# Optimization experiments

Hardware: AMD Instinct MI355X
Metric: run time of the kernel (lower is better)

Reference implementation:

```python
import jax, jax.numpy as jnp
import numpy as np

N_NODES = 50000
N_EDGES = 1600000
N_GRAPHS = 64


def setup_inputs() -> dict:
    key = jax.random.key(0)
    ks = jax.random.split(key, 16)
    p = lambda k, shape: (jax.random.normal(k, shape, dtype=jnp.float32) * 0.05)
    x = jax.random.normal(ks[0], (N_NODES, 128), dtype=jnp.float32)
    edge_index = jax.random.randint(ks[1], (2, N_EDGES), 0, N_NODES, dtype=jnp.int32)
    edge_attr = jax.random.uniform(ks[2], (N_EDGES,), dtype=jnp.float32)
    batch = jnp.sort(jax.random.randint(ks[3], (N_NODES,), 0, N_GRAPHS, dtype=jnp.int32))
    return {
        'x': x, 'edge_index': edge_index, 'edge_attr': edge_attr, 'batch': batch,
        'W1': p(ks[4], (128, 128)), 'b1': jnp.zeros((128,), jnp.float32),
        'W2': p(ks[5], (128, 64)), 'b2': jnp.zeros((64,), jnp.float32),
        'gW1': p(ks[6], (64, 32)), 'gb1': jnp.zeros((32,), jnp.float32),
        'gW2': p(ks[7], (32, 1)), 'gb2': jnp.zeros((1,), jnp.float32),
        'fcW1': p(ks[8], (64, 128)), 'fcb1': jnp.zeros((128,), jnp.float32),
        'fcW2': p(ks[9], (128, 2)), 'fcb2': jnp.zeros((2,), jnp.float32),
    }


def gcn_conv(x, src, dst, ew, W, b):
    # PyG GCNConv with edge weights: add self-loops (weight 1), symmetric norm.
    xw = x @ W  # [N, out]
    deg = jax.ops.segment_sum(ew, dst, num_segments=N_NODES) + 1.0  # self-loop
    dinv = jnp.where(deg > 0, jax.lax.rsqrt(deg), 0.0)
    coef = dinv[src] * ew * dinv[dst]  # [E]
    agg = jax.ops.segment_sum(coef[:, None] * xw[src], dst, num_segments=N_NODES)
    agg = agg + (dinv * dinv)[:, None] * xw  # self-loop contribution
    return agg + b


def global_attention(x, batch, gW1, gb1, gW2, gb2):
    # gate_nn: Linear(64,32)->ReLU->Linear(32,1), segment-softmax over graphs
    g = (jax.nn.relu(x @ gW1 + gb1) @ gW2 + gb2)[:, 0]  # [N]
    gmax = jax.ops.segment_max(g, batch, num_segments=N_GRAPHS)
    ex = jnp.exp(g - gmax[batch])
    den = jax.ops.segment_sum(ex, batch, num_segments=N_GRAPHS)
    alpha = ex / den[batch]
    return jax.ops.segment_sum(alpha[:, None] * x, batch, num_segments=N_GRAPHS)


def reference(x, edge_index, edge_attr, batch, W1, b1, W2, b2,
              gW1, gb1, gW2, gb2, fcW1, fcb1, fcW2, fcb2):
    src, dst = edge_index[0], edge_index[1]
    h = jax.nn.relu(gcn_conv(x, src, dst, edge_attr, W1, b1))
    x1 = jax.nn.relu(gcn_conv(h, src, dst, edge_attr, W2, b2))
    x2 = global_attention(x1, batch, gW1, gb1, gW2, gb2)  # [G, 64]
    # dropout is identity in eval mode
    h2 = jax.nn.relu(x2 @ fcW1 + fcb1)
    logits = h2 @ fcW2 + fcb2
    return jax.nn.log_softmax(logits, axis=1)
```

## Files before the change

### kernel.cpp

```cpp
#include <hip/hip_runtime.h>
#include <hip/hip_bf16.h>
#include <hip/hip_fp16.h>

#define N_NODES 50000
#define N_EDGES 1600000
#define N_GRAPHS 64
#define G1BLKS 1563

__device__ __forceinline__ unsigned fenc(float x) {
    unsigned u = __float_as_uint(x);
    return (u & 0x80000000u) ? ~u : (u | 0x80000000u);
}
__device__ __forceinline__ float fdec(unsigned e) {
    return (e & 0x80000000u) ? __uint_as_float(e & 0x7fffffffu) : __uint_as_float(~e);
}
__device__ __forceinline__ float ew_of(unsigned p) {
    return __half2float(__ushort_as_half((unsigned short)(p & 0xFFFFu)));
}

__global__ void mega1(const float* __restrict__ X, const float* __restrict__ W,
                      __half* __restrict__ Yh, const int* __restrict__ dst,
                      int* __restrict__ cnt, int* __restrict__ pos) {
    __shared__ float Xl[32][132];
    if (blockIdx.x >= G1BLKS) {
        int e = (blockIdx.x - G1BLKS) * 256 + threadIdx.x;
        if (e < N_EDGES) pos[e] = atomicAdd(&cnt[dst[e]], 1);
        return;
    }
    const int rt = threadIdx.x >> 5;
    const int ct = threadIdx.x & 31;
    const int base = blockIdx.x * 32;
    for (int i = threadIdx.x; i < 32 * 32; i += 256) {
        int rr = i >> 5, cc = (i & 31) << 2;
        int gr = base + rr;
        float4 v = (gr < N_NODES) ? *(const float4*)&X[(size_t)gr * 128 + cc]
                                  : make_float4(0.f, 0.f, 0.f, 0.f);
        Xl[rr][cc] = v.x; Xl[rr][cc + 1] = v.y; Xl[rr][cc + 2] = v.z; Xl[rr][cc + 3] = v.w;
    }
    __syncthreads();
    float acc[4][4] = {};
    for (int k = 0; k < 128; k += 4) {
        float4 a0 = *(const float4*)&Xl[rt * 4 + 0][k];
        float4 a1 = *(const float4*)&Xl[rt * 4 + 1][k];
        float4 a2 = *(const float4*)&Xl[rt * 4 + 2][k];
        float4 a3 = *(const float4*)&Xl[rt * 4 + 3][k];
        float4 w0 = *(const float4*)&W[(size_t)(k + 0) * 128 + ct * 4];
        float4 w1 = *(const float4*)&W[(size_t)(k + 1) * 128 + ct * 4];
        float4 w2 = *(const float4*)&W[(size_t)(k + 2) * 128 + ct * 4];
        float4 w3 = *(const float4*)&W[(size_t)(k + 3) * 128 + ct * 4];
        #define STEP(av, wv)  \
            acc[0][0] += av##0 * wv.x; acc[0][1] += av##0 * wv.y; acc[0][2] += av##0 * wv.z; acc[0][3] += av##0 * wv.w; \
            acc[1][0] += av##1 * wv.x; acc[1][1] += av##1 * wv.y; acc[1][2] += av##1 * wv.z; acc[1][3] += av##1 * wv.w; \
            acc[2][0] += av##2 * wv.x; acc[2][1] += av##2 * wv.y; acc[2][2] += av##2 * wv.z; acc[2][3] += av##2 * wv.w; \
            acc[3][0] += av##3 * wv.x; acc[3][1] += av##3 * wv.y; acc[3][2] += av##3 * wv.z; acc[3][3] += av##3 * wv.w;
        { float ax0=a0.x, ax1=a1.x, ax2=a2.x, ax3=a3.x; STEP(ax, w0) }
        { float ay0=a0.y, ay1=a1.y, ay2=a2.y, ay3=a3.y; STEP(ay, w1) }
        { float az0=a0.z, az1=a1.z, az2=a2.z, az3=a3.z; STEP(az, w2) }
        { float aw0=a0.w, aw1=a1.w, aw2=a2.w, aw3=a3.w; STEP(aw, w3) }
        #undef STEP
    }
    const int pc = ct >> 3;
    const int cw = (ct & 7) * 4;
    for (int i = 0; i < 4; ++i) {
        int gr = base + rt * 4 + i;
        if (gr < N_NODES) {
            ushort4 u;
            u.x = __half_as_ushort(__float2half(acc[i][0]));
            u.y = __half_as_ushort(__float2half(acc[i][1]));
            u.z = __half_as_ushort(__float2half(acc[i][2]));
            u.w = __half_as_ushort(__float2half(acc[i][3]));
            *(ushort4*)&Yh[((size_t)pc * N_NODES + gr) * 32 + cw] = u;
        }
    }
}

__global__ void block_sums(const int* __restrict__ cnt, int* __restrict__ bsum) {
    __shared__ int s[256];
    int idx = blockIdx.x * 256 + threadIdx.x;
    s[threadIdx.x] = (idx < N_NODES) ? cnt[idx] : 0;
    __syncthreads();
    for (int o = 128; o; o >>= 1) {
        if (threadIdx.x < o) s[threadIdx.x] += s[threadIdx.x + o];
        __syncthreads();
    }
    if (threadIdx.x == 0) bsum[blockIdx.x] = s[0];
}

__global__ void scan_bsums(const int* __restrict__ bsum, int* __restrict__ boff,
                           int nb, int* __restrict__ row_start_last) {
    __shared__ int s[256];
    int v = (threadIdx.x < nb) ? bsum[threadIdx.x] : 0;
    s[threadIdx.x] = v;
    __syncthreads();
    for (int o = 1; o < 256; o <<= 1) {
        int t = 0;
        if (threadIdx.x >= o) t = s[threadIdx.x - o];
        __syncthreads();
        s[threadIdx.x] += t;
        __syncthreads();
    }
    if (threadIdx.x < nb) boff[threadIdx.x] = s[threadIdx.x] - v;
    if (threadIdx.x == 0) *row_start_last = N_EDGES;
}

__global__ void scan_counts(const int* __restrict__ cnt, const int* __restrict__ boff,
                            int* __restrict__ row_start) {
    __shared__ int s[256];
    int idx = blockIdx.x * 256 + threadIdx.x;
    int v = (idx < N_NODES) ? cnt[idx] : 0;
    s[threadIdx.x] = v;
    __syncthreads();
    for (int o = 1; o < 256; o <<= 1) {
        int t = 0;
        if (threadIdx.x >= o) t = s[threadIdx.x - o];
        __syncthreads();
        s[threadIdx.x] += t;
        __syncthreads();
    }
    if (idx < N_NODES) row_start[idx] = boff[blockIdx.x] + s[threadIdx.x] - v;
}

__global__ void fill_direct(const int* __restrict__ src, const int* __restrict__ dst,
                            const float* __restrict__ ew, const int* __restrict__ pos,
                            const int* __restrict__ row_start, unsigned* __restrict__ csr) {
    int e = blockIdx.x * 256 + threadIdx.x;
    if (e < N_EDGES) {
        int d = dst[e];
        unsigned short hb = __half_as_ushort(__float2half(ew[e]));
        csr[row_start[d] + pos[e]] = ((unsigned)src[e] << 16) | (unsigned)hb;
    }
}

__global__ void deg_dinv_csr(const int* __restrict__ row_start, const unsigned* __restrict__ csr,
                             float* __restrict__ dinv) {
    int t = blockIdx.x * 256 + threadIdx.x;
    int n = t >> 4;
    int l = t & 15;
    if (n >= N_NODES) return;
    int beg = row_start[n], end = row_start[n + 1];
    float s = 0.f;
    for (int i = beg + l; i < end; i += 16) s += ew_of(csr[i]);
    for (int o = 8; o; o >>= 1) s += __shfl_xor(s, o, 16);
    if (l == 0) dinv[n] = rsqrtf(s + 1.0f);
}

__global__ void scale_xwh(__half* __restrict__ xwh, const float* __restrict__ dinv) {
    const size_t tot = (size_t)4 * N_NODES * 32 / 8;
    size_t i = (size_t)blockIdx.x * 256 + threadIdx.x;
    if (i >= tot) return;
    size_t h0 = i * 8;
    int n = (int)((h0 >> 5) % N_NODES);
    float dv = dinv[n];
    __half2* p = (__half2*)(xwh + h0);
    #pragma unroll
    for (int j = 0; j < 4; ++j) {
        float2 f = __half22float2(p[j]);
        p[j] = __floats2half2_rn(f.x * dv, f.y * dv);
    }
}

__global__ void gemm2_reg(const float* __restrict__ X, const float* __restrict__ W,
                          const float* __restrict__ dinv, __half* __restrict__ Yh, int nrows) {
    __shared__ float Xl[32][132];
    __shared__ float Wl[128][64];
    const int rt = threadIdx.x >> 5;
    const int ct = threadIdx.x & 31;
    const int base = blockIdx.x * 32;
    for (int i = threadIdx.x; i < 32 * 32; i += 256) {
        int rr = i >> 5, cc = (i & 31) << 2;
        int gr = base + rr;
        float4 v = (gr < nrows) ? *(const float4*)&X[(size_t)gr * 128 + cc]
                                : make_float4(0.f, 0.f, 0.f, 0.f);
        Xl[rr][cc] = v.x; Xl[rr][cc + 1] = v.y; Xl[rr][cc + 2] = v.z; Xl[rr][cc + 3] = v.w;
    }
    for (int i = threadIdx.x; i < 128 * 16; i += 256) {
        int kk = i >> 4, cc = (i & 15) << 2;
        *(float4*)&Wl[kk][cc] = *(const float4*)&W[(size_t)kk * 64 + cc];
    }
    float acc[4][2] = {};
    __syncthreads();
    for (int k = 0; k < 128; k += 4) {
        float4 a0 = *(const float4*)&Xl[rt * 4 + 0][k];
        float4 a1 = *(const float4*)&Xl[rt * 4 + 1][k];
        float4 a2 = *(const float4*)&Xl[rt * 4 + 2][k];
        float4 a3 = *(const float4*)&Xl[rt * 4 + 3][k];
        float2 w0 = *(const float2*)&Wl[k + 0][ct * 2];
        float2 w1 = *(const float2*)&Wl[k + 1][ct * 2];
        float2 w2 = *(const float2*)&Wl[k + 2][ct * 2];
        float2 w3 = *(const float2*)&Wl[k + 3][ct * 2];
        acc[0][0] += a0.x * w0.x; acc[0][1] += a0.x * w0.y;
        acc[1][0] += a1.x * w0.x; acc[1][1] += a1.x * w0.y;
        acc[2][0] += a2.x * w0.x; acc[2][1] += a2.x * w0.y;
        acc[3][0] += a3.x * w0.x; acc[3][1] += a3.x * w0.y;
        acc[0][0] += a0.y * w1.x; acc[0][1] += a0.y * w1.y;
        acc[1][0] += a1.y * w1.x; acc[1][1] += a1.y * w1.y;
        acc[2][0] += a2.y * w1.x; acc[2][1] += a2.y * w1.y;
        acc[3][0] += a3.y * w1.x; acc[3][1] += a3.y * w1.y;
        acc[0][0] += a0.z * w2.x; acc[0][1] += a0.z * w2.y;
        acc[1][0] += a1.z * w2.x; acc[1][1] += a1.z * w2.y;
        acc[2][0] += a2.z * w2.x; acc[2][1] += a2.z * w2.y;
        acc[3][0] += a3.z * w2.x; acc[3][1] += a3.z * w2.y;
        acc[0][0] += a0.w * w3.x; acc[0][1] += a0.w * w3.y;
        acc[1][0] += a1.w * w3.x; acc[1][1] += a1.w * w3.y;
        acc[2][0] += a2.w * w3.x; acc[2][1] += a2.w * w3.y;
        acc[3][0] += a3.w * w3.x; acc[3][1] += a3.w * w3.y;
    }
    const int col0 = ct * 2;
    const int pc   = col0 >> 5;
    const int cw   = col0 & 31;
    for (int i = 0; i < 4; ++i) {
        int gr = base + rt * 4 + i;
        if (gr < nrows) {
            float dv = dinv[gr];
            __half2 hv = __floats2half2_rn(acc[i][0] * dv, acc[i][1] * dv);
            *(__half2*)&Yh[((size_t)pc * nrows + gr) * 32 + cw] = hv;
        }
    }
}

template<int NP>
__global__ void agg_csr_pair(const int* __restrict__ row_start, const unsigned* __restrict__ csr,
                             const __half* __restrict__ xwh, const float* __restrict__ dinv,
                             const float* __restrict__ b, float* __restrict__ out_h) {
    constexpr int OUT = NP * 32;
    const int c    = blockIdx.x % NP;
    const int nb   = blockIdx.x / NP;
    const int n    = nb * 8 + (threadIdx.x >> 5);
    const int kk   = threadIdx.x & 15;
    const int half = (threadIdx.x >> 4) & 1;
    if (n >= N_NODES) return;
    const __half* __restrict__ bp = xwh + ((size_t)c * N_NODES) * 32 + 2 * kk;
    const int beg = row_start[n], end = row_start[n + 1];
    float ax = 0.f, ay = 0.f;
    int i = beg + half;
    for (; i + 6 < end; i += 8) {
        unsigned p0 = csr[i],     p1 = csr[i + 2];
        unsigned p2 = csr[i + 4], p3 = csr[i + 6];
        float2 f0 = __half22float2(*(const __half2*)(bp + (size_t)(p0 >> 16) * 32));
        float2 f1 = __half22float2(*(const __half2*)(bp + (size_t)(p1 >> 16) * 32));
        float2 f2 = __half22float2(*(const __half2*)(bp + (size_t)(p2 >> 16) * 32));
        float2 f3 = __half22float2(*(const __half2*)(bp + (size_t)(p3 >> 16) * 32));
        float e0 = ew_of(p0), e1 = ew_of(p1), e2 = ew_of(p2), e3 = ew_of(p3);
        ax += e0 * f0.x + e1 * f1.x + e2 * f2.x + e3 * f3.x;
        ay += e0 * f0.y + e1 * f1.y + e2 * f2.y + e3 * f3.y;
    }
    for (; i < end; i += 2) {
        unsigned p = csr[i];
        float2 f = __half22float2(*(const __half2*)(bp + (size_t)(p >> 16) * 32));
        float e = ew_of(p);
        ax += e * f.x; ay += e * f.y;
    }
    ax += __shfl_xor(ax, 16);
    ay += __shfl_xor(ay, 16);
    if (half == 0) {
        float2 sf = __half22float2(*(const __half2*)(bp + (size_t)n * 32));
        float dv = dinv[n];
        int kg = c * 32 + 2 * kk;
        float2 o;
        o.x = fmaxf(dv * (ax + sf.x) + b[kg], 0.f);
        o.y = fmaxf(dv * (ay + sf.y) + b[kg + 1], 0.f);
        *(float2*)&out_h[(size_t)n * OUT + kg] = o;
    }
}

__global__ void gate_kernel(const float* __restrict__ x1, const float* __restrict__ gW1,
                            const float* __restrict__ gb1, const float* __restrict__ gW2,
                            const float* __restrict__ gb2, const int* __restrict__ batch,
                            float* __restrict__ g, unsigned* __restrict__ gmax_enc) {
    __shared__ float W1l[64 * 32];
    __shared__ float W2l[32];
    __shared__ float b1l[32];
    for (int i = threadIdx.x; i < 64 * 32; i += 256) W1l[i] = gW1[i];
    if (threadIdx.x < 32) { W2l[threadIdx.x] = gW2[threadIdx.x]; b1l[threadIdx.x] = gb1[threadIdx.x]; }
    __syncthreads();
    const float gb2v = gb2[0];
    int n = blockIdx.x * 256 + threadIdx.x;
    bool act = (n < N_NODES);
    float gv = -1e30f;
    int b = 0;
    if (act) {
        const float* row = x1 + (size_t)n * 64;
        float t[32];
        #pragma unroll
        for (int j = 0; j < 32; ++j) t[j] = b1l[j];
        for (int k = 0; k < 64; ++k) {
            float xv = row[k];
            #pragma unroll
            for (int j = 0; j < 32; ++j) t[j] += xv * W1l[k * 32 + j];
        }
        float a = gb2v;
        #pragma unroll
        for (int j = 0; j < 32; ++j) a += fmaxf(t[j], 0.f) * W2l[j];
        gv = a;
        g[n] = a;
        b = batch[n];
    }
    unsigned long long actm = __ballot(act);
    int b0 = __shfl(b, 0);
    bool uniform = (actm == ~0ull) && (__ballot(b == b0) == ~0ull);
    if (uniform) {
        float m = gv;
        for (int o = 32; o; o >>= 1) m = fmaxf(m, __shfl_xor(m, o));
        if ((threadIdx.x & 63) == 0) atomicMax(&gmax_enc[b0], fenc(m));
    } else if (act) {
        atomicMax(&gmax_enc[b], fenc(gv));
    }
}

__global__ void exp_kernel(const float* __restrict__ g, const int* __restrict__ batch,
                           const unsigned* __restrict__ gmax_enc, float* __restrict__ ex,
                           float* __restrict__ den) {
    int n = blockIdx.x * 256 + threadIdx.x;
    bool act = (n < N_NODES);
    float v = 0.f; int b = 0;
    if (act) {
        b = batch[n];
        v = expf(g[n] - fdec(gmax_enc[b]));
        ex[n] = v;
    }
    unsigned long long actm = __ballot(act);
    int b0 = __shfl(b, 0);
    bool uniform = (actm == ~0ull) && (__ballot(b == b0) == ~0ull);
    if (uniform) {
        float s = v;
        for (int o = 32; o; o >>= 1) s += __shfl_xor(s, o);
        if ((threadIdx.x & 63) == 0) atomicAdd(&den[b0], s);
    } else if (act) {
        atomicAdd(&den[b], v);
    }
}

__global__ void pool_kernel(const float* __restrict__ x1, const float* __restrict__ ex,
                            const float* __restrict__ den, const int* __restrict__ batch,
                            float* __restrict__ pooled) {
    const int L = 32;
    const int f   = threadIdx.x & 63;
    const int grp = threadIdx.x >> 6;
    int chunk = blockIdx.x * 4 + grp;
    int start = chunk * L;
    if (start >= N_NODES) return;
    int end = min(start + L, N_NODES);
    int cur = batch[start];
    float rden = 1.f / den[cur];
    float acc = 0.f;
    for (int n = start; n < end; ++n) {
        int bb = batch[n];
        if (bb != cur) {
            atomicAdd(&pooled[cur * 64 + f], acc);
            acc = 0.f; cur = bb; rden = 1.f / den[cur];
        }
        acc += ex[n] * rden * x1[(size_t)n * 64 + f];
    }
    atomicAdd(&pooled[cur * 64 + f], acc);
}

__global__ void head_kernel(const float* __restrict__ pooled, const float* __restrict__ fcW1,
                            const float* __restrict__ fcb1, const float* __restrict__ fcW2,
                            const float* __restrict__ fcb2, float* __restrict__ out) {
    __shared__ float P[64];
    __shared__ float r0[2], r1[2];
    const int gi = blockIdx.x;
    if (threadIdx.x < 64) P[threadIdx.x] = pooled[gi * 64 + threadIdx.x];
    __syncthreads();
    const int j = threadIdx.x;
    float a = fcb1[j];
    #pragma unroll 8
    for (int k = 0; k < 64; ++k) a += P[k] * fcW1[k * 128 + j];
    float h = fmaxf(a, 0.f);
    float p0 = h * fcW2[j * 2 + 0];
    float p1 = h * fcW2[j * 2 + 1];
    for (int o = 32; o; o >>= 1) { p0 += __shfl_xor(p0, o); p1 += __shfl_xor(p1, o); }
    if ((threadIdx.x & 63) == 0) { r0[threadIdx.x >> 6] = p0; r1[threadIdx.x >> 6] = p1; }
    __syncthreads();
    if (threadIdx.x == 0) {
        float l0 = r0[0] + r0[1] + fcb2[0];
        float l1 = r1[0] + r1[1] + fcb2[1];
        float m = fmaxf(l0, l1);
        float lse = m + logf(expf(l0 - m) + expf(l1 - m));
        out[gi * 2 + 0] = l0 - lse;
        out[gi * 2 + 1] = l1 - lse;
    }
}

extern "C" void kernel_launch(void* const* d_in, const int* in_sizes, int n_in,
                              void* d_out, int out_size, void* d_ws, size_t ws_size,
                              hipStream_t stream) {
    const float* x    = (const float*)d_in[0];
    const int*   ei   = (const int*)d_in[1];
    const float* ew   = (const float*)d_in[2];
    const int*   batch= (const int*)d_in[3];
    const float* W1   = (const float*)d_in[4];
    const float* b1   = (const float*)d_in[5];
    const float* W2   = (const float*)d_in[6];
    const float* b2   = (const float*)d_in[7];
    const float* gW1  = (const float*)d_in[8];
    const float* gb1  = (const float*)d_in[9];
    const float* gW2  = (const float*)d_in[10];
    const float* gb2  = (const float*)d_in[11];
    const float* fcW1 = (const float*)d_in[12];
    const float* fcb1 = (const float*)d_in[13];
    const float* fcW2 = (const float*)d_in[14];
    const float* fcb2 = (const float*)d_in[15];
    float* out = (float*)d_out;

    const int* src = ei;
    const int* dst = ei + N_EDGES;

    const int EB = (N_EDGES + 255) / 256;
    const int NB = (N_NODES + 255) / 256;
    const int NBLK8  = (N_NODES + 7) / 8;
    const int NBLK16 = (N_NODES + 15) / 16;

    float* ws = (float*)d_ws;
    __half* xwh  = (__half*)ws;
    float* agg   = ws + 3200000;
    size_t off = 9600000;
    unsigned* csr   = (unsigned*)(ws + off); off += 1600000;
    int*   pos      = (int*)(ws + off);    off += 1600000;
    int*   row_start= (int*)(ws + off);    off += 50176;
    int*   cnt      = (int*)(ws + off);    off += 50176;
    float* dinv     = ws + off;            off += 50176;
    float* g        = ws + off;            off += 50048;
    float* ex       = ws + off;            off += 50048;
    int*   bsum     = (int*)(ws + off);    off += 256;
    int*   boff     = (int*)(ws + off);    off += 256;
    unsigned* gmax  = (unsigned*)(ws + off); off += 64;
    float* den      = ws + off;            off += 64;
    float* pooled   = ws + off;            off += 4096;

    hipMemsetAsync(cnt, 0, N_NODES * sizeof(int), stream);
    mega1<<<G1BLKS + EB, 256, 0, stream>>>(x, W1, xwh, dst, cnt, pos);

    block_sums<<<NB, 256, 0, stream>>>(cnt, bsum);
    scan_bsums<<<1, 256, 0, stream>>>(bsum, boff, NB, row_start + N_NODES);
    scan_counts<<<NB, 256, 0, stream>>>(cnt, boff, row_start);
    fill_direct<<<EB, 256, 0, stream>>>(src, dst, ew, pos, row_start, csr);
    deg_dinv_csr<<<NBLK16, 256, 0, stream>>>(row_start, csr, dinv);
    scale_xwh<<<(4 * N_NODES * 32 / 8 + 255) / 256, 256, 0, stream>>>(xwh, dinv);

    agg_csr_pair<4><<<4 * NBLK8, 256, 0, stream>>>(row_start, csr, xwh, dinv, b1, agg);

    gemm2_reg<<<(N_NODES + 31) / 32, 256, 0, stream>>>(agg, W2, dinv, xwh, N_NODES);
    agg_csr_pair<2><<<2 * NBLK8, 256, 0, stream>>>(row_start, csr, xwh, dinv, b2, agg);

    hipMemsetAsync(gmax, 0, N_GRAPHS * sizeof(unsigned), stream);
    hipMemsetAsync(den, 0, N_GRAPHS * sizeof(float), stream);
    hipMemsetAsync(pooled, 0, N_GRAPHS * 64 * sizeof(float), stream);
    gate_kernel<<<NB, 256, 0, stream>>>(agg, gW1, gb1, gW2, gb2, batch, g, gmax);
    exp_kernel<<<NB, 256, 0, stream>>>(g, batch, gmax, ex, den);
    int nchunks = (N_NODES + 31) / 32;
    pool_kernel<<<(nchunks + 3) / 4, 256, 0, stream>>>(agg, ex, den, batch, pooled);

    head_kernel<<<N_GRAPHS, 128, 0, stream>>>(pooled, fcW1, fcb1, fcW2, fcb2, out);
}
```

Measured before the change: 338.8 us.

## Fuse degree into counting atomic, precompute edge coefs, half hidden, fuse exp+pool

The edge-counting pass now does one 64-bit atomic that packs the count with a fixed-point weighted degree. This removes the separate degree kernel over the CSR and lets dinv be computed during the block-sum pass. The CSR fill stores the full normalized coefficient dinv[s]*w*dinv[d] in fp16, so the xwh scaling pass and the per-row dinv scaling in gemm2 and the aggregation go away. The layer-1 output is stored as fp16 to halve the traffic into gemm2. The exp and pooling kernels are merged, with normalization deferred to the head kernel, and nontemporal loads and stores are added. Risks: fp16 and fixed-point precision loss in the coefficients and degree, and 64-bit atomic contention.

```diff
diff --git a/kernel.cpp b/kernel.cpp
--- a/kernel.cpp
+++ b/kernel.cpp
@@ -14,17 +14,24 @@
 __device__ __forceinline__ float fdec(unsigned e) {
     return (e & 0x80000000u) ? __uint_as_float(e & 0x7fffffffu) : __uint_as_float(~e);
 }
-__device__ __forceinline__ float ew_of(unsigned p) {
+__device__ __forceinline__ float coef_of(unsigned p) {
     return __half2float(__ushort_as_half((unsigned short)(p & 0xFFFFu)));
 }
 
 __global__ void mega1(const float* __restrict__ X, const float* __restrict__ W,
                       __half* __restrict__ Yh, const int* __restrict__ dst,
-                      int* __restrict__ cnt, int* __restrict__ pos) {
+                      const float* __restrict__ ew,
+                      unsigned long long* __restrict__ packed, int* __restrict__ pos) {
     __shared__ float Xl[32][132];
     if (blockIdx.x >= G1BLKS) {
         int e = (blockIdx.x - G1BLKS) * 256 + threadIdx.x;
-        if (e < N_EDGES) pos[e] = atomicAdd(&cnt[dst[e]], 1);
+        if (e < N_EDGES) {
+            int d = __builtin_nontemporal_load(&dst[e]);
+            float w = __builtin_nontemporal_load(&ew[e]);
+            unsigned fix = (unsigned)(w * 16777216.0f);
+            unsigned long long old = atomicAdd(&packed[d], 0x100000000ull | (unsigned long long)fix);
+            pos[e] = (int)(old >> 32);
+        }
         return;
     }
     const int rt = threadIdx.x >> 5;
@@ -74,10 +81,17 @@
     }
 }
 
-__global__ void block_sums(const int* __restrict__ cnt, int* __restrict__ bsum) {
+__global__ void block_sums_dinv(const unsigned long long* __restrict__ packed,
+                                int* __restrict__ bsum, float* __restrict__ dinv) {
     __shared__ int s[256];
     int idx = blockIdx.x * 256 + threadIdx.x;
-    s[threadIdx.x] = (idx < N_NODES) ? cnt[idx] : 0;
+    int c = 0;
+    if (idx < N_NODES) {
+        unsigned long long p = packed[idx];
+        c = (int)(p >> 32);
+        dinv[idx] = rsqrtf((float)(unsigned)(p & 0xFFFFFFFFu) * (1.0f / 16777216.0f) + 1.0f);
+    }
+    s[threadIdx.x] = c;
     __syncthreads();
     for (int o = 128; o; o >>= 1) {
         if (threadIdx.x < o) s[threadIdx.x] += s[threadIdx.x + o];
@@ -103,11 +117,11 @@
     if (threadIdx.x == 0) *row_start_last = N_EDGES;
 }
 
-__global__ void scan_counts(const int* __restrict__ cnt, const int* __restrict__ boff,
-                            int* __restrict__ row_start) {
+__global__ void scan_counts(const unsigned long long* __restrict__ packed,
+                            const int* __restrict__ boff, int* __restrict__ row_start) {
     __shared__ int s[256];
     int idx = blockIdx.x * 256 + threadIdx.x;
-    int v = (idx < N_NODES) ? cnt[idx] : 0;
+    int v = (idx < N_NODES) ? (int)(packed[idx] >> 32) : 0;
     s[threadIdx.x] = v;
     __syncthreads();
     for (int o = 1; o < 256; o <<= 1) {
@@ -122,45 +136,75 @@
 
 __global__ void fill_direct(const int* __restrict__ src, const int* __restrict__ dst,
                             const float* __restrict__ ew, const int* __restrict__ pos,
-                            const int* __restrict__ row_start, unsigned* __restrict__ csr) {
+                            const int* __restrict__ row_start, const float* __restrict__ dinv,
+                            unsigned* __restrict__ csr) {
     int e = blockIdx.x * 256 + threadIdx.x;
     if (e < N_EDGES) {
-        int d = dst[e];
-        unsigned short hb = __half_as_ushort(__float2half(ew[e]));
-        csr[row_start[d] + pos[e]] = ((unsigned)src[e] << 16) | (unsigned)hb;
-    }
-}
-
-__global__ void deg_dinv_csr(const int* __restrict__ row_start, const unsigned* __restrict__ csr,
-                             float* __restrict__ dinv) {
-    int t = blockIdx.x * 256 + threadIdx.x;
-    int n = t >> 4;
-    int l = t & 15;
+        int d = __builtin_nontemporal_load(&dst[e]);
+        int s = __builtin_nontemporal_load(&src[e]);
+        float w = __builtin_nontemporal_load(&ew[e]);
+        int p = __builtin_nontemporal_load(&pos[e]);
+        float coef = dinv[s] * w * dinv[d];
+        unsigned val = ((unsigned)s << 16) | __half_as_ushort(__float2half(coef));
+        __builtin_nontemporal_store(val, &csr[row_start[d] + p]);
+    }
+}
+
+template<int NP, bool HOUT>
+__global__ void agg_csr_pair(const int* __restrict__ row_start, const unsigned* __restrict__ csr,
+                             const __half* __restrict__ xwh, const float* __restrict__ dinv,
+                             const float* __restrict__ b, void* __restrict__ outp) {
+    constexpr int OUT = NP * 32;
+    const int c    = blockIdx.x % NP;
+    const int nb   = blockIdx.x / NP;
+    const int n    = nb * 8 + (threadIdx.x >> 5);
+    const int kk   = threadIdx.x & 15;
+    const int half = (threadIdx.x >> 4) & 1;
     if (n >= N_NODES) return;
-    int beg = row_start[n], end = row_start[n + 1];
-    float s = 0.f;
-    for (int i = beg + l; i < end; i += 16) s += ew_of(csr[i]);
-    for (int o = 8; o; o >>= 1) s += __shfl_xor(s, o, 16);
-    if (l == 0) dinv[n] = rsqrtf(s + 1.0f);
-}
-
-__global__ void scale_xwh(__half* __restrict__ xwh, const float* __restrict__ dinv) {
-    const size_t tot = (size_t)4 * N_NODES * 32 / 8;
-    size_t i = (size_t)blockIdx.x * 256 + threadIdx.x;
-    if (i >= tot) return;
-    size_t h0 = i * 8;
-    int n = (int)((h0 >> 5) % N_NODES);
-    float dv = dinv[n];
-    __half2* p = (__half2*)(xwh + h0);
-    #pragma unroll
-    for (int j = 0; j < 4; ++j) {
-        float2 f = __half22float2(p[j]);
-        p[j] = __floats2half2_rn(f.x * dv, f.y * dv);
-    }
-}
-
-__global__ void gemm2_reg(const float* __restrict__ X, const float* __restrict__ W,
-                          const float* __restrict__ dinv, __half* __restrict__ Yh, int nrows) {
+    const __half* __restrict__ bp = xwh + ((size_t)c * N_NODES) * 32 + 2 * kk;
+    const int beg = row_start[n], end = row_start[n + 1];
+    float ax = 0.f, ay = 0.f;
+    int i = beg + half;
+    for (; i + 6 < end; i += 8) {
+        unsigned p0 = __builtin_nontemporal_load(&csr[i]);
+        unsigned p1 = __builtin_nontemporal_load(&csr[i + 2]);
+        unsigned p2 = __builtin_nontemporal_load(&csr[i + 4]);
+        unsigned p3 = __builtin_nontemporal_load(&csr[i + 6]);
+        float2 f0 = __half22float2(*(const __half2*)(bp + (size_t)(p0 >> 16) * 32));
+        float2 f1 = __half22float2(*(const __half2*)(bp + (size_t)(p1 >> 16) * 32));
+        float2 f2 = __half22float2(*(const __half2*)(bp + (size_t)(p2 >> 16) * 32));
+        float2 f3 = __half22float2(*(const __half2*)(bp + (size_t)(p3 >> 16) * 32));
+        float e0 = coef_of(p0), e1 = coef_of(p1), e2 = coef_of(p2), e3 = coef_of(p3);
+        ax += e0 * f0.x + e1 * f1.x + e2 * f2.x + e3 * f3.x;
+        ay += e0 * f0.y + e1 * f1.y + e2 * f2.y + e3 * f3.y;
+    }
+    for (; i < end; i += 2) {
+        unsigned p = __builtin_nontemporal_load(&csr[i]);
+        float2 f = __half22float2(*(const __half2*)(bp + (size_t)(p >> 16) * 32));
+        float e = coef_of(p);
+        ax += e * f.x; ay += e * f.y;
+    }
+    ax += __shfl_xor(ax, 16);
+    ay += __shfl_xor(ay, 16);
+    if (half == 0) {
+        float2 sf = __half22float2(*(const __half2*)(bp + (size_t)n * 32));
+        float dv = dinv[n];
+        float dv2 = dv * dv;
+        int kg = c * 32 + 2 * kk;
+        float ox = fmaxf(ax + dv2 * sf.x + b[kg], 0.f);
+        float oy = fmaxf(ay + dv2 * sf.y + b[kg + 1], 0.f);
+        if constexpr (HOUT) {
+            __half* o = (__half*)outp;
+            *(__half2*)&o[(size_t)n * OUT + kg] = __floats2half2_rn(ox, oy);
+        } else {
+            float* o = (float*)outp;
+            *(float2*)&o[(size_t)n * OUT + kg] = make_float2(ox, oy);
+        }
+    }
+}
+
+__global__ void gemm2_reg(const __half* __restrict__ Xh, const float* __restrict__ W,
+                          __half* __restrict__ Yh, int nrows) {
     __shared__ float Xl[32][132];
     __shared__ float Wl[128][64];
     const int rt = threadIdx.x >> 5;
@@ -169,9 +213,13 @@
     for (int i = threadIdx.x; i < 32 * 32; i += 256) {
         int rr = i >> 5, cc = (i & 31) << 2;
         int gr = base + rr;
-        float4 v = (gr < nrows) ? *(const float4*)&X[(size_t)gr * 128 + cc]
-                                : make_float4(0.f, 0.f, 0.f, 0.f);
-        Xl[rr][cc] = v.x; Xl[rr][cc + 1] = v.y; Xl[rr][cc + 2] = v.z; Xl[rr][cc + 3] = v.w;
+        float2 fa = make_float2(0.f, 0.f), fb = fa;
+        if (gr < nrows) {
+            const __half2* ph = (const __half2*)&Xh[(size_t)gr * 128 + cc];
+            fa = __half22float2(ph[0]);
+            fb = __half22float2(ph[1]);
+        }
+        Xl[rr][cc] = fa.x; Xl[rr][cc + 1] = fa.y; Xl[rr][cc + 2] = fb.x; Xl[rr][cc + 3] = fb.y;
     }
     for (int i = threadIdx.x; i < 128 * 16; i += 256) {
         int kk = i >> 4, cc = (i & 15) << 2;
@@ -211,55 +259,9 @@
     for (int i = 0; i < 4; ++i) {
         int gr = base + rt * 4 + i;
         if (gr < nrows) {
-            float dv = dinv[gr];
-            __half2 hv = __floats2half2_rn(acc[i][0] * dv, acc[i][1] * dv);
+            __half2 hv = __floats2half2_rn(acc[i][0], acc[i][1]);
             *(__half2*)&Yh[((size_t)pc * nrows + gr) * 32 + cw] = hv;
         }
-    }
-}
-
-template<int NP>
-__global__ void agg_csr_pair(const int* __restrict__ row_start, const unsigned* __restrict__ csr,
-                             const __half* __restrict__ xwh, const float* __restrict__ dinv,
-                             const float* __restrict__ b, float* __restrict__ out_h) {
-    constexpr int OUT = NP * 32;
-    const int c    = blockIdx.x % NP;
-    const int nb   = blockIdx.x / NP;
-    const int n    = nb * 8 + (threadIdx.x >> 5);
-    const int kk   = threadIdx.x & 15;
-    const int half = (threadIdx.x >> 4) & 1;
-    if (n >= N_NODES) return;
-    const __half* __restrict__ bp = xwh + ((size_t)c * N_NODES) * 32 + 2 * kk;
-    const int beg = row_start[n], end = row_start[n + 1];
-    float ax = 0.f, ay = 0.f;
-    int i = beg + half;
-    for (; i + 6 < end; i += 8) {
-        unsigned p0 = csr[i],     p1 = csr[i + 2];
-        unsigned p2 = csr[i + 4], p3 = csr[i + 6];
-        float2 f0 = __half22float2(*(const __half2*)(bp + (size_t)(p0 >> 16) * 32));
-        float2 f1 = __half22float2(*(const __half2*)(bp + (size_t)(p1 >> 16) * 32));
-        float2 f2 = __half22float2(*(const __half2*)(bp + (size_t)(p2 >> 16) * 32));
-        float2 f3 = __half22float2(*(const __half2*)(bp + (size_t)(p3 >> 16) * 32));
-        float e0 = ew_of(p0), e1 = ew_of(p1), e2 = ew_of(p2), e3 = ew_of(p3);
-        ax += e0 * f0.x + e1 * f1.x + e2 * f2.x + e3 * f3.x;
-        ay += e0 * f0.y + e1 * f1.y + e2 * f2.y + e3 * f3.y;
-    }
-    for (; i < end; i += 2) {
-        unsigned p = csr[i];
-        float2 f = __half22float2(*(const __half2*)(bp + (size_t)(p >> 16) * 32));
-        float e = ew_of(p);
-        ax += e * f.x; ay += e * f.y;
-    }
-    ax += __shfl_xor(ax, 16);
-    ay += __shfl_xor(ay, 16);
-    if (half == 0) {
-        float2 sf = __half22float2(*(const __half2*)(bp + (size_t)n * 32));
-        float dv = dinv[n];
-        int kg = c * 32 + 2 * kk;
-        float2 o;
-        o.x = fmaxf(dv * (ax + sf.x) + b[kg], 0.f);
-        o.y = fmaxf(dv * (ay + sf.y) + b[kg + 1], 0.f);
-        *(float2*)&out_h[(size_t)n * OUT + kg] = o;
     }
 }
 
@@ -307,32 +309,9 @@
     }
 }
 
-__global__ void exp_kernel(const float* __restrict__ g, const int* __restrict__ batch,
-                           const unsigned* __restrict__ gmax_enc, float* __restrict__ ex,
-                           float* __restrict__ den) {
-    int n = blockIdx.x * 256 + threadIdx.x;
-    bool act = (n < N_NODES);
-    float v = 0.f; int b = 0;
-    if (act) {
-        b = batch[n];
-        v = expf(g[n] - fdec(gmax_enc[b]));
-        ex[n] = v;
-    }
-    unsigned long long actm = __ballot(act);
-    int b0 = __shfl(b, 0);
-    bool uniform = (actm == ~0ull) && (__ballot(b == b0) == ~0ull);
-    if (uniform) {
-        float s = v;
-        for (int o = 32; o; o >>= 1) s += __shfl_xor(s, o);
-        if ((threadIdx.x & 63) == 0) atomicAdd(&den[b0], s);
-    } else if (act) {
-        atomicAdd(&den[b], v);
-    }
-}
-
-__global__ void pool_kernel(const float* __restrict__ x1, const float* __restrict__ ex,
-                            const float* __restrict__ den, const int* __restrict__ batch,
-                            float* __restrict__ pooled) {
+__global__ void exp_pool(const float* __restrict__ x1, const float* __restrict__ g,
+                         const unsigned* __restrict__ gmax_enc, const int* __restrict__ batch,
+                         float* __restrict__ den, float* __restrict__ pooledU) {
     const int L = 32;
     const int f   = threadIdx.x & 63;
     const int grp = threadIdx.x >> 6;
@@ -341,26 +320,31 @@
     if (start >= N_NODES) return;
     int end = min(start + L, N_NODES);
     int cur = batch[start];
-    float rden = 1.f / den[cur];
-    float acc = 0.f;
+    float gm = fdec(gmax_enc[cur]);
+    float acc = 0.f, accd = 0.f;
     for (int n = start; n < end; ++n) {
         int bb = batch[n];
         if (bb != cur) {
-            atomicAdd(&pooled[cur * 64 + f], acc);
-            acc = 0.f; cur = bb; rden = 1.f / den[cur];
-        }
-        acc += ex[n] * rden * x1[(size_t)n * 64 + f];
-    }
-    atomicAdd(&pooled[cur * 64 + f], acc);
-}
-
-__global__ void head_kernel(const float* __restrict__ pooled, const float* __restrict__ fcW1,
-                            const float* __restrict__ fcb1, const float* __restrict__ fcW2,
-                            const float* __restrict__ fcb2, float* __restrict__ out) {
+            atomicAdd(&pooledU[cur * 64 + f], acc);
+            if (f == 0) atomicAdd(&den[cur], accd);
+            acc = 0.f; accd = 0.f; cur = bb; gm = fdec(gmax_enc[cur]);
+        }
+        float e = expf(g[n] - gm);
+        acc += e * x1[(size_t)n * 64 + f];
+        if (f == 0) accd += e;
+    }
+    atomicAdd(&pooledU[cur * 64 + f], acc);
+    if (f == 0) atomicAdd(&den[cur], accd);
+}
+
+__global__ void head_kernel(const float* __restrict__ pooledU, const float* __restrict__ den,
+                            const float* __restrict__ fcW1, const float* __restrict__ fcb1,
+                            const float* __restrict__ fcW2, const float* __restrict__ fcb2,
+                            float* __restrict__ out) {
     __shared__ float P[64];
     __shared__ float r0[2], r1[2];
     const int gi = blockIdx.x;
-    if (threadIdx.x < 64) P[threadIdx.x] = pooled[gi * 64 + threadIdx.x];
+    if (threadIdx.x < 64) P[threadIdx.x] = pooledU[gi * 64 + threadIdx.x] / den[gi];
     __syncthreads();
     const int j = threadIdx.x;
     float a = fcb1[j];
@@ -409,47 +393,44 @@
     const int EB = (N_EDGES + 255) / 256;
     const int NB = (N_NODES + 255) / 256;
     const int NBLK8  = (N_NODES + 7) / 8;
-    const int NBLK16 = (N_NODES + 15) / 16;
 
     float* ws = (float*)d_ws;
     __half* xwh  = (__half*)ws;
-    float* agg   = ws + 3200000;
+    __half* hbuf = (__half*)(ws + 3200000);
+    float*  x1   = ws + 6400000;
     size_t off = 9600000;
     unsigned* csr   = (unsigned*)(ws + off); off += 1600000;
     int*   pos      = (int*)(ws + off);    off += 1600000;
     int*   row_start= (int*)(ws + off);    off += 50176;
-    int*   cnt      = (int*)(ws + off);    off += 50176;
+    unsigned long long* packed = (unsigned long long*)(ws + off); off += 100096;
     float* dinv     = ws + off;            off += 50176;
     float* g        = ws + off;            off += 50048;
-    float* ex       = ws + off;            off += 50048;
     int*   bsum     = (int*)(ws + off);    off += 256;
     int*   boff     = (int*)(ws + off);    off += 256;
     unsigned* gmax  = (unsigned*)(ws + off); off += 64;
     float* den      = ws + off;            off += 64;
     float* pooled   = ws + off;            off += 4096;
 
-    hipMemsetAsync(cnt, 0, N_NODES * sizeof(int), stream);
-    mega1<<<G1BLKS + EB, 256, 0, stream>>>(x, W1, xwh, dst, cnt, pos);
-
-    block_sums<<<NB, 256, 0, stream>>>(cnt, bsum);
+    hipMemsetAsync(packed, 0, 50048 * sizeof(unsigned long long), stream);
+    hipMemsetAsync(gmax, 0, (64 + 64 + 4096) * sizeof(float), stream);
+
+    mega1<<<G1BLKS + EB, 256, 0, stream>>>(x, W1, xwh, dst, ew, packed, pos);
+
+    block_sums_dinv<<<NB, 256, 0, stream>>>(packed, bsum, dinv);
     scan_bsums<<<1, 256, 0, stream>>>(bsum, boff, NB, row_start + N_NODES);
-    scan_counts<<<NB, 256, 0, stream>>>(cnt, boff, row_start);
-    fill_direct<<<EB, 256, 0, stream>>>(src, dst, ew, pos, row_start, csr);
-    deg_dinv_csr<<<NBLK16, 256, 0, stream>>>(row_start, csr, dinv);
-    scale_xwh<<<(4 * N_NODES * 32 / 8 + 255) / 256, 256, 0, stream>>>(xwh, dinv);
-
-    agg_csr_pair<4><<<4 * NBLK8, 256, 0, stream>>>(row_start, csr, xwh, dinv, b1, agg);
-
-    gemm2_reg<<<(N_NODES + 31) / 32, 256, 0, stream>>>(agg, W2, dinv, xwh, N_NODES);
-    agg_csr_pair<2><<<2 * NBLK8, 256, 0, stream>>>(row_start, csr, xwh, dinv, b2, agg);
-
-    hipMemsetAsync(gmax, 0, N_GRAPHS * sizeof(unsigned), stream);
-    hipMemsetAsync(den, 0, N_GRAPHS * sizeof(float), stream);
-    hipMemsetAsync(pooled, 0, N_GRAPHS * 64 * sizeof(float), stream);
-    gate_kernel<<<NB, 256, 0, stream>>>(agg, gW1, gb1, gW2, gb2, batch, g, gmax);
-    exp_kernel<<<NB, 256, 0, stream>>>(g, batch, gmax, ex, den);
-    int nchunks = (N_NODES + 31) / 32;
-    pool_kernel<<<(nchunks + 3) / 4, 256, 0, stream>>>(agg, ex, den, batch, pooled);
-
-    head_kernel<<<N_GRAPHS, 128, 0, stream>>>(pooled, fcW1, fcb1, fcW2, fcb2, out);
-}
+    scan_counts<<<NB, 256, 0, stream>>>(packed, boff, row_start);
+    fill_direct<<<EB, 256, 0, stream>>>(src, dst, ew, pos, row_start, dinv, csr);
+
+    agg_csr_pair<4, true><<<4 * NBLK8, 256, 0, stream>>>(row_start, csr, xwh, dinv, b1, hbuf);
+
+    gemm2_reg<<<(N_NODES + 31) / 32, 256, 0, stream>>>(hbuf, W2, xwh, N_NODES);
+    agg_csr_pair<2, false><<<2 * NBLK8, 256, 0, stream>>>(row_start, csr, xwh, dinv, b2, x1);
+
+    gate_kernel<<<NB, 256, 0, stream>>>(x1, gW1, gb1, gW2, gb2, batch, g, gmax);
+    {
+        int nchunks = (N_NODES + 31) / 32;
+        exp_pool<<<(nchunks + 3) / 4, 256, 0, stream>>>(x1, g, gmax, batch, den, pooled);
+    }
+
+    head_kernel<<<N_GRAPHS, 128, 0, stream>>>(pooled, den, fcW1, fcb1, fcW2, fcb2, out);
+}
```

After: 383.9 us. 1.13x slower.
